# Optimization experiments

Hardware: AMD Instinct MI355X
Metric: run time of the kernel (lower is better)

Reference implementation:

```python
import jax, jax.numpy as jnp
import numpy as np

HEADS = 4

def setup_inputs() -> dict:
    B, L, D = 4, 2048, 256
    key = jax.random.key(0)
    k1, k2, k3, k4, k5, k6 = jax.random.split(key, 6)
    return {
        "atten": jax.random.normal(k1, (B, L, L), dtype=jnp.float32),
        "value": jax.random.normal(k2, (B, L, D), dtype=jnp.float32),
        "mask": jax.random.uniform(k3, (B, 1, L, L), dtype=jnp.float32),
        "padding_mask": jax.random.randint(k4, (B, L, L), 0, 2, dtype=jnp.int32),
        "Wv": jax.random.normal(k5, (D, D), dtype=jnp.float32) * 0.02,
        "bv": jnp.zeros((D,), dtype=jnp.float32),
        "Wo": jax.random.normal(k6, (D, D), dtype=jnp.float32) * 0.02,
        "bo": jnp.zeros((D,), dtype=jnp.float32),
    }

def reference(atten, value, mask, padding_mask, Wv, bv, Wo, bo):
    B, L, D = value.shape
    H = HEADS
    dk = D // H
    # to_value: Linear then split heads. N == 1 (value.unsqueeze(1) in torch).
    v = value @ Wv + bv                                   # (B, L, D)
    v = v.reshape(B, 1, L, H, dk).transpose(0, 3, 1, 2, 4)  # (B, H, N=1, L, dk)
    # externally supplied attention logits, two sequential masked fills
    a = atten[:, None, :, :]                              # (B, 1, L, L)
    a = jnp.where(mask < 0.5, jnp.finfo(a.dtype).min, a)
    a = jnp.where(padding_mask[:, None, :, :] == 0, -jnp.inf, a)
    a = jax.nn.softmax(a, axis=-1)                        # (B, 1, L, L)
    # dropout is identity in eval mode
    # einsum 'bhij,bhnjk->bhnik' with h=1 on a broadcast across H heads of v
    out = jnp.einsum('bij,bhnjk->bhnik', a[:, 0], v)      # (B, H, 1, L, dk)
    out = out.transpose(0, 2, 3, 1, 4).reshape(B, 1, L, D)
    out = out @ Wo + bo                                   # (B, 1, L, D)
    return out
```

## Files before the change

kernel.cpp:

```cpp
#include <hip/hip_runtime.h>
#include <hip/hip_bf16.h>
#include <math.h>

#define L 2048
#define D 256
#define NEG_FLT_MAX (-3.402823466e38f)

typedef __attribute__((ext_vector_type(8))) short bf16x8;
typedef __attribute__((ext_vector_type(4))) float f32x4;
typedef __attribute__((ext_vector_type(4))) int i32x4;

__device__ __forceinline__ unsigned short f2bf(float f) {
    union { float f; unsigned int u; } v; v.f = f;
    unsigned int r = v.u + 0x7FFFu + ((v.u >> 16) & 1u);
    return (unsigned short)(r >> 16);
}

__global__ __launch_bounds__(256, 4) void prep_kernel(
    const float* __restrict__ value, const float* __restrict__ Wv,
    const float* __restrict__ bv, const float* __restrict__ Wo,
    unsigned short* __restrict__ Vt, unsigned short* __restrict__ Wot) {
    const int tid = threadIdx.x;
    const int wave = tid >> 6, lane = tid & 63;
    const int lm = lane & 15, q = lane >> 4;
    const int rh = wave >> 1;
    const int nh = wave & 1;
    const int m0 = blockIdx.x * 32;
    const int n0 = blockIdx.y * 64;

    __shared__ __align__(16) unsigned short Wlds[64][264];

    {
        int bid = blockIdx.y * 256 + blockIdx.x;
        if (tid < 64) {
            int e = bid * 64 + tid;
            int k = e >> 8, n = e & 255;
            Wot[n * 256 + k] = f2bf(Wo[k * 256 + n]);
        }
    }

    {
        int krow = tid >> 4;
        int nrel = (tid & 15) * 4;
#pragma unroll
        for (int p = 0; p < 16; p++) {
            int k = p * 16 + krow;
            f32x4 w = *reinterpret_cast<const f32x4*>(Wv + (size_t)k * 256 + n0 + nrel);
            Wlds[nrel + 0][k] = f2bf(w[0]);
            Wlds[nrel + 1][k] = f2bf(w[1]);
            Wlds[nrel + 2][k] = f2bf(w[2]);
            Wlds[nrel + 3][k] = f2bf(w[3]);
        }
    }
    __syncthreads();

    const int nl0 = nh * 32 + lm;
    const int nl1 = nh * 32 + 16 + lm;
    const int arow = m0 + rh * 16 + lm;

    f32x4 acc[2];
    acc[0] = (f32x4)(0.f); acc[1] = (f32x4)(0.f);

    const float* ap = value + (size_t)arow * 256;
    f32x4 pa0 = *reinterpret_cast<const f32x4*>(ap + q * 8);
    f32x4 pa1 = *reinterpret_cast<const f32x4*>(ap + q * 8 + 4);

    for (int k0 = 0; k0 < 256; k0 += 32) {
        f32x4 a0 = pa0, a1 = pa1;
        if (k0 < 224) {
            int kq = k0 + 32 + q * 8;
            pa0 = *reinterpret_cast<const f32x4*>(ap + kq);
            pa1 = *reinterpret_cast<const f32x4*>(ap + kq + 4);
        }
        bf16x8 b0 = *reinterpret_cast<const bf16x8*>(&Wlds[nl0][k0 + q * 8]);
        bf16x8 b1 = *reinterpret_cast<const bf16x8*>(&Wlds[nl1][k0 + q * 8]);
        bf16x8 afr;
#pragma unroll
        for (int e = 0; e < 4; e++) afr[e] = (short)f2bf(a0[e]);
#pragma unroll
        for (int e = 0; e < 4; e++) afr[4 + e] = (short)f2bf(a1[e]);
        acc[0] = __builtin_amdgcn_mfma_f32_16x16x32_bf16(afr, b0, acc[0], 0, 0, 0);
        acc[1] = __builtin_amdgcn_mfma_f32_16x16x32_bf16(afr, b1, acc[1], 0, 0, 0);
    }

    int mrow = m0 + rh * 16 + q * 4;
    int b = mrow >> 11;
    int j = mrow & 2047;
#pragma unroll
    for (int nf = 0; nf < 2; nf++) {
        int n = n0 + nh * 32 + nf * 16 + lm;
        float bias_n = bv[n];
        const f32x4& a = acc[nf];
        unsigned short* dst = Vt + (size_t)b * (D * L) + (size_t)n * L + j;
        ushort4 pk;
        pk.x = f2bf(a[0] + bias_n);
        pk.y = f2bf(a[1] + bias_n);
        pk.z = f2bf(a[2] + bias_n);
        pk.w = f2bf(a[3] + bias_n);
        *reinterpret_cast<ushort4*>(dst) = pk;
    }
}

__global__ __launch_bounds__(256, 2) void attn_kernel(
    const float* __restrict__ atten, const float* __restrict__ mask,
    const int* __restrict__ pad, const unsigned short* __restrict__ Vt,
    const unsigned short* __restrict__ Wot, const float* __restrict__ bo,
    float* __restrict__ out) {
    const int g = blockIdx.x;
    const int b = g >> 7;
    const int i0 = (g & 127) * 16;
    const int tid = threadIdx.x;
    const int wave = tid >> 6, lane = tid & 63;
    const int lm = lane & 15, q = lane >> 4;
    const int r = tid >> 4;
    const int c = (tid & 15) * 8;

    __shared__ __align__(16) unsigned short Plds[2][16][136];
    __shared__ __align__(16) unsigned short A_lds[16][264];
    __shared__ float l_lds[16];

    f32x4 acc[4];
#pragma unroll
    for (int nf = 0; nf < 4; nf++) acc[nf] = (f32x4)(0.f);
    float lsum = 0.f;

    const size_t rowoff = ((size_t)(b * L + i0 + r)) * L + c;
    const float* at_p = atten + rowoff;
    const float* mk_p = mask + rowoff;
    const int*   pd_p = pad + rowoff;
    const unsigned short* vt_b = Vt + (size_t)b * (D * L);

    f32x4 pa0 = *reinterpret_cast<const f32x4*>(at_p);
    f32x4 pa1 = *reinterpret_cast<const f32x4*>(at_p + 4);
    f32x4 pm0 = *reinterpret_cast<const f32x4*>(mk_p);
    f32x4 pm1 = *reinterpret_cast<const f32x4*>(mk_p + 4);
    i32x4 pp0 = *reinterpret_cast<const i32x4*>(pd_p);
    i32x4 pp1 = *reinterpret_cast<const i32x4*>(pd_p + 4);

    for (int jt = 0; jt < 16; jt++) {
        const int j0 = jt * 128;
        bf16x8 bfr[4][4];
#pragma unroll
        for (int kk = 0; kk < 4; kk++)
#pragma unroll
            for (int nf = 0; nf < 4; nf++) {
                int n = wave * 64 + nf * 16 + lm;
                bfr[kk][nf] = *reinterpret_cast<const bf16x8*>(
                    vt_b + (size_t)n * L + j0 + kk * 32 + q * 8);
            }
        f32x4 a0 = pa0, a1 = pa1, k0 = pm0, k1 = pm1;
        i32x4 p0 = pp0, p1 = pp1;
        if (jt < 15) {
            pa0 = *reinterpret_cast<const f32x4*>(at_p + j0 + 128);
            pa1 = *reinterpret_cast<const f32x4*>(at_p + j0 + 132);
            pm0 = *reinterpret_cast<const f32x4*>(mk_p + j0 + 128);
            pm1 = *reinterpret_cast<const f32x4*>(mk_p + j0 + 132);
            pp0 = *reinterpret_cast<const i32x4*>(pd_p + j0 + 128);
            pp1 = *reinterpret_cast<const i32x4*>(pd_p + j0 + 132);
        }
        bf16x8 pk;
#pragma unroll
        for (int e = 0; e < 4; e++) {
            float sv = (k0[e] < 0.5f) ? NEG_FLT_MAX : a0[e];
            sv = (p0[e] == 0) ? -INFINITY : sv;
            float pv = __expf(sv);
            lsum += pv;
            pk[e] = (short)f2bf(pv);
            float sw = (k1[e] < 0.5f) ? NEG_FLT_MAX : a1[e];
            sw = (p1[e] == 0) ? -INFINITY : sw;
            float pw = __expf(sw);
            lsum += pw;
            pk[4 + e] = (short)f2bf(pw);
        }
        const int par = jt & 1;
        *reinterpret_cast<bf16x8*>(&Plds[par][r][c]) = pk;
        __syncthreads();

#pragma unroll
        for (int kk = 0; kk < 4; kk++) {
            bf16x8 afr = *reinterpret_cast<const bf16x8*>(
                &Plds[par][lm][kk * 32 + q * 8]);
#pragma unroll
            for (int nf = 0; nf < 4; nf++)
                acc[nf] = __builtin_amdgcn_mfma_f32_16x16x32_bf16(
                    afr, bfr[kk][nf], acc[nf], 0, 0, 0);
        }
    }

    lsum += __shfl_xor(lsum, 1);
    lsum += __shfl_xor(lsum, 2);
    lsum += __shfl_xor(lsum, 4);
    lsum += __shfl_xor(lsum, 8);
    if ((tid & 15) == 0) l_lds[r] = lsum;
    __syncthreads();

    float linv[4];
#pragma unroll
    for (int rg = 0; rg < 4; rg++) linv[rg] = 1.f / l_lds[q * 4 + rg];
#pragma unroll
    for (int nf = 0; nf < 4; nf++) {
        int n = wave * 64 + nf * 16 + lm;
#pragma unroll
        for (int rg = 0; rg < 4; rg++)
            A_lds[q * 4 + rg][n] = f2bf(acc[nf][rg] * linv[rg]);
    }
    __syncthreads();

    f32x4 oacc[4];
#pragma unroll
    for (int nf = 0; nf < 4; nf++) oacc[nf] = (f32x4)(0.f);
    for (int k0 = 0; k0 < 256; k0 += 32) {
        bf16x8 afr = *reinterpret_cast<const bf16x8*>(&A_lds[lm][k0 + q * 8]);
#pragma unroll
        for (int nf = 0; nf < 4; nf++) {
            int n = wave * 64 + nf * 16 + lm;
            bf16x8 bfrW = *reinterpret_cast<const bf16x8*>(
                Wot + (size_t)n * 256 + k0 + q * 8);
            oacc[nf] = __builtin_amdgcn_mfma_f32_16x16x32_bf16(
                afr, bfrW, oacc[nf], 0, 0, 0);
        }
    }
#pragma unroll
    for (int nf = 0; nf < 4; nf++) {
        int n = wave * 64 + nf * 16 + lm;
        float bias_n = bo[n];
#pragma unroll
        for (int rg = 0; rg < 4; rg++)
            out[((size_t)(b * L + i0 + q * 4 + rg)) * 256 + n] = oacc[nf][rg] + bias_n;
    }
}

extern "C" void kernel_launch(void* const* d_in, const int* in_sizes, int n_in,
                              void* d_out, int out_size, void* d_ws, size_t ws_size,
                              hipStream_t stream) {
    (void)in_sizes; (void)n_in; (void)out_size; (void)ws_size;
    const float* atten = (const float*)d_in[0];
    const float* value = (const float*)d_in[1];
    const float* mask  = (const float*)d_in[2];
    const int*   pad   = (const int*)d_in[3];
    const float* Wv    = (const float*)d_in[4];
    const float* bv    = (const float*)d_in[5];
    const float* Wo    = (const float*)d_in[6];
    const float* bo    = (const float*)d_in[7];
    float* out = (float*)d_out;

    char* ws = (char*)d_ws;
    unsigned short* Vt  = (unsigned short*)(ws);
    unsigned short* Wot = (unsigned short*)(ws + 4194304);

    prep_kernel<<<dim3(256, 4), 256, 0, stream>>>(value, Wv, bv, Wo, Vt, Wot);
    attn_kernel<<<512, 256, 0, stream>>>(atten, mask, pad, Vt, Wot, bo, out);
}
```

Before: 254.1 us.

## Double-buffer V fragments in registers and remap blocks across batches

Unrolls the key-tile loop by two with A/B register sets, so the V fragments and next-tile attention/mask/pad loads for tile j+1 are issued before the MFMA work of tile j, rather than the V loads sitting directly ahead of their own MFMAs. It also remaps the block index so consecutive blocks land on different batches, changing L2/XCD locality. This raises register pressure (two 4x4 bf16x8 fragment arrays), which could reduce occupancy under launch_bounds(256,2).

Result: faster. 248.3 us (-2.3%).

```diff
diff --git a/kernel.cpp b/kernel.cpp
--- a/kernel.cpp
+++ b/kernel.cpp
@@ -106,7 +106,8 @@
     const int* __restrict__ pad, const unsigned short* __restrict__ Vt,
     const unsigned short* __restrict__ Wot, const float* __restrict__ bo,
     float* __restrict__ out) {
-    const int g = blockIdx.x;
+    const int bid = blockIdx.x;
+    const int g = (bid & 7) * 64 + (bid >> 3);
     const int b = g >> 7;
     const int i0 = (g & 127) * 16;
     const int tid = threadIdx.x;
@@ -128,62 +129,117 @@
     const float* at_p = atten + rowoff;
     const float* mk_p = mask + rowoff;
     const int*   pd_p = pad + rowoff;
-    const unsigned short* vt_b = Vt + (size_t)b * (D * L);
-
-    f32x4 pa0 = *reinterpret_cast<const f32x4*>(at_p);
-    f32x4 pa1 = *reinterpret_cast<const f32x4*>(at_p + 4);
-    f32x4 pm0 = *reinterpret_cast<const f32x4*>(mk_p);
-    f32x4 pm1 = *reinterpret_cast<const f32x4*>(mk_p + 4);
-    i32x4 pp0 = *reinterpret_cast<const i32x4*>(pd_p);
-    i32x4 pp1 = *reinterpret_cast<const i32x4*>(pd_p + 4);
-
-    for (int jt = 0; jt < 16; jt++) {
-        const int j0 = jt * 128;
-        bf16x8 bfr[4][4];
-#pragma unroll
-        for (int kk = 0; kk < 4; kk++)
-#pragma unroll
-            for (int nf = 0; nf < 4; nf++) {
-                int n = wave * 64 + nf * 16 + lm;
-                bfr[kk][nf] = *reinterpret_cast<const bf16x8*>(
-                    vt_b + (size_t)n * L + j0 + kk * 32 + q * 8);
-            }
-        f32x4 a0 = pa0, a1 = pa1, k0 = pm0, k1 = pm1;
-        i32x4 p0 = pp0, p1 = pp1;
-        if (jt < 15) {
-            pa0 = *reinterpret_cast<const f32x4*>(at_p + j0 + 128);
-            pa1 = *reinterpret_cast<const f32x4*>(at_p + j0 + 132);
-            pm0 = *reinterpret_cast<const f32x4*>(mk_p + j0 + 128);
-            pm1 = *reinterpret_cast<const f32x4*>(mk_p + j0 + 132);
-            pp0 = *reinterpret_cast<const i32x4*>(pd_p + j0 + 128);
-            pp1 = *reinterpret_cast<const i32x4*>(pd_p + j0 + 132);
-        }
-        bf16x8 pk;
-#pragma unroll
-        for (int e = 0; e < 4; e++) {
-            float sv = (k0[e] < 0.5f) ? NEG_FLT_MAX : a0[e];
-            sv = (p0[e] == 0) ? -INFINITY : sv;
-            float pv = __expf(sv);
-            lsum += pv;
-            pk[e] = (short)f2bf(pv);
-            float sw = (k1[e] < 0.5f) ? NEG_FLT_MAX : a1[e];
-            sw = (p1[e] == 0) ? -INFINITY : sw;
-            float pw = __expf(sw);
-            lsum += pw;
-            pk[4 + e] = (short)f2bf(pw);
-        }
-        const int par = jt & 1;
-        *reinterpret_cast<bf16x8*>(&Plds[par][r][c]) = pk;
-        __syncthreads();
-
-#pragma unroll
-        for (int kk = 0; kk < 4; kk++) {
-            bf16x8 afr = *reinterpret_cast<const bf16x8*>(
-                &Plds[par][lm][kk * 32 + q * 8]);
-#pragma unroll
-            for (int nf = 0; nf < 4; nf++)
-                acc[nf] = __builtin_amdgcn_mfma_f32_16x16x32_bf16(
-                    afr, bfr[kk][nf], acc[nf], 0, 0, 0);
+    const unsigned short* vt_b = Vt + (size_t)b * (D * L) + q * 8;
+
+    f32x4 laA0, laA1, lmA0, lmA1, laB0, laB1, lmB0, lmB1;
+    i32x4 lpA0, lpA1, lpB0, lpB1;
+    bf16x8 bfrA[4][4], bfrB[4][4];
+
+    laA0 = *reinterpret_cast<const f32x4*>(at_p);
+    laA1 = *reinterpret_cast<const f32x4*>(at_p + 4);
+    lmA0 = *reinterpret_cast<const f32x4*>(mk_p);
+    lmA1 = *reinterpret_cast<const f32x4*>(mk_p + 4);
+    lpA0 = *reinterpret_cast<const i32x4*>(pd_p);
+    lpA1 = *reinterpret_cast<const i32x4*>(pd_p + 4);
+#pragma unroll
+    for (int kk = 0; kk < 4; kk++)
+#pragma unroll
+        for (int nf = 0; nf < 4; nf++) {
+            int n = wave * 64 + nf * 16 + lm;
+            bfrA[kk][nf] = *reinterpret_cast<const bf16x8*>(
+                vt_b + (size_t)n * L + kk * 32);
+        }
+
+    for (int jt = 0; jt < 16; jt += 2) {
+        {
+            const int j0 = jt * 128;
+            bf16x8 pk;
+#pragma unroll
+            for (int e = 0; e < 4; e++) {
+                float sv = (lmA0[e] < 0.5f) ? NEG_FLT_MAX : laA0[e];
+                sv = (lpA0[e] == 0) ? -INFINITY : sv;
+                float pv = __expf(sv);
+                lsum += pv;
+                pk[e] = (short)f2bf(pv);
+                float sw = (lmA1[e] < 0.5f) ? NEG_FLT_MAX : laA1[e];
+                sw = (lpA1[e] == 0) ? -INFINITY : sw;
+                float pw = __expf(sw);
+                lsum += pw;
+                pk[4 + e] = (short)f2bf(pw);
+            }
+            *reinterpret_cast<bf16x8*>(&Plds[0][r][c]) = pk;
+            {
+                const int jn = j0 + 128;
+                laB0 = *reinterpret_cast<const f32x4*>(at_p + jn);
+                laB1 = *reinterpret_cast<const f32x4*>(at_p + jn + 4);
+                lmB0 = *reinterpret_cast<const f32x4*>(mk_p + jn);
+                lmB1 = *reinterpret_cast<const f32x4*>(mk_p + jn + 4);
+                lpB0 = *reinterpret_cast<const i32x4*>(pd_p + jn);
+                lpB1 = *reinterpret_cast<const i32x4*>(pd_p + jn + 4);
+#pragma unroll
+                for (int kk = 0; kk < 4; kk++)
+#pragma unroll
+                    for (int nf = 0; nf < 4; nf++) {
+                        int n = wave * 64 + nf * 16 + lm;
+                        bfrB[kk][nf] = *reinterpret_cast<const bf16x8*>(
+                            vt_b + (size_t)n * L + jn + kk * 32);
+                    }
+            }
+            __syncthreads();
+#pragma unroll
+            for (int kk = 0; kk < 4; kk++) {
+                bf16x8 afr = *reinterpret_cast<const bf16x8*>(
+                    &Plds[0][lm][kk * 32 + q * 8]);
+#pragma unroll
+                for (int nf = 0; nf < 4; nf++)
+                    acc[nf] = __builtin_amdgcn_mfma_f32_16x16x32_bf16(
+                        afr, bfrA[kk][nf], acc[nf], 0, 0, 0);
+            }
+        }
+        {
+            const int j0 = jt * 128 + 128;
+            bf16x8 pk;
+#pragma unroll
+            for (int e = 0; e < 4; e++) {
+                float sv = (lmB0[e] < 0.5f) ? NEG_FLT_MAX : laB0[e];
+                sv = (lpB0[e] == 0) ? -INFINITY : sv;
+                float pv = __expf(sv);
+                lsum += pv;
+                pk[e] = (short)f2bf(pv);
+                float sw = (lmB1[e] < 0.5f) ? NEG_FLT_MAX : laB1[e];
+                sw = (lpB1[e] == 0) ? -INFINITY : sw;
+                float pw = __expf(sw);
+                lsum += pw;
+                pk[4 + e] = (short)f2bf(pw);
+            }
+            *reinterpret_cast<bf16x8*>(&Plds[1][r][c]) = pk;
+            if (jt < 14) {
+                const int jn = j0 + 128;
+                laA0 = *reinterpret_cast<const f32x4*>(at_p + jn);
+                laA1 = *reinterpret_cast<const f32x4*>(at_p + jn + 4);
+                lmA0 = *reinterpret_cast<const f32x4*>(mk_p + jn);
+                lmA1 = *reinterpret_cast<const f32x4*>(mk_p + jn + 4);
+                lpA0 = *reinterpret_cast<const i32x4*>(pd_p + jn);
+                lpA1 = *reinterpret_cast<const i32x4*>(pd_p + jn + 4);
+#pragma unroll
+                for (int kk = 0; kk < 4; kk++)
+#pragma unroll
+                    for (int nf = 0; nf < 4; nf++) {
+                        int n = wave * 64 + nf * 16 + lm;
+                        bfrA[kk][nf] = *reinterpret_cast<const bf16x8*>(
+                            vt_b + (size_t)n * L + jn + kk * 32);
+                    }
+            }
+            __syncthreads();
+#pragma unroll
+            for (int kk = 0; kk < 4; kk++) {
+                bf16x8 afr = *reinterpret_cast<const bf16x8*>(
+                    &Plds[1][lm][kk * 32 + q * 8]);
+#pragma unroll
+                for (int nf = 0; nf < 4; nf++)
+                    acc[nf] = __builtin_amdgcn_mfma_f32_16x16x32_bf16(
+                        afr, bfrB[kk][nf], acc[nf], 0, 0, 0);
+            }
         }
     }
 
```

## Use single-wave blocks with register-direct P fragments and double-buffered prefetch

Applied to the files above, without the earlier changes.

The attention kernel now runs one 64-thread wave per block, covering all 256 output columns for 16 rows. The softmax numerators are built directly in the MFMA A-fragment layout, so the shared-memory staging of P and the per-tile __syncthreads are gone. Logits, masks and V fragments are double-buffered in registers, one 32-column step ahead. The cost is only 512 waves across the GPU and heavy register use (16 accumulators plus two 16-fragment V buffers), which lowers occupancy and leaves less parallelism to hide memory latency.

Result: slower. 284.7 us (+12.0%).

```diff
diff --git a/kernel.cpp b/kernel.cpp
--- a/kernel.cpp
+++ b/kernel.cpp
@@ -101,7 +101,7 @@
     }
 }
 
-__global__ __launch_bounds__(256, 2) void attn_kernel(
+__global__ __launch_bounds__(64, 1) void attn_kernel(
     const float* __restrict__ atten, const float* __restrict__ mask,
     const int* __restrict__ pad, const unsigned short* __restrict__ Vt,
     const unsigned short* __restrict__ Wot, const float* __restrict__ bo,
@@ -109,120 +109,138 @@
     const int g = blockIdx.x;
     const int b = g >> 7;
     const int i0 = (g & 127) * 16;
-    const int tid = threadIdx.x;
-    const int wave = tid >> 6, lane = tid & 63;
+    const int lane = threadIdx.x & 63;
     const int lm = lane & 15, q = lane >> 4;
-    const int r = tid >> 4;
-    const int c = (tid & 15) * 8;
-
-    __shared__ __align__(16) unsigned short Plds[2][16][136];
+
     __shared__ __align__(16) unsigned short A_lds[16][264];
     __shared__ float l_lds[16];
 
-    f32x4 acc[4];
-#pragma unroll
-    for (int nf = 0; nf < 4; nf++) acc[nf] = (f32x4)(0.f);
+    f32x4 acc[16];
+#pragma unroll
+    for (int nf = 0; nf < 16; nf++) acc[nf] = (f32x4)(0.f);
     float lsum = 0.f;
 
-    const size_t rowoff = ((size_t)(b * L + i0 + r)) * L + c;
+    const size_t rowoff = ((size_t)(b * L + i0 + lm)) * L + q * 8;
     const float* at_p = atten + rowoff;
     const float* mk_p = mask + rowoff;
     const int*   pd_p = pad + rowoff;
-    const unsigned short* vt_b = Vt + (size_t)b * (D * L);
-
-    f32x4 pa0 = *reinterpret_cast<const f32x4*>(at_p);
-    f32x4 pa1 = *reinterpret_cast<const f32x4*>(at_p + 4);
-    f32x4 pm0 = *reinterpret_cast<const f32x4*>(mk_p);
-    f32x4 pm1 = *reinterpret_cast<const f32x4*>(mk_p + 4);
-    i32x4 pp0 = *reinterpret_cast<const i32x4*>(pd_p);
-    i32x4 pp1 = *reinterpret_cast<const i32x4*>(pd_p + 4);
-
-    for (int jt = 0; jt < 16; jt++) {
-        const int j0 = jt * 128;
-        bf16x8 bfr[4][4];
-#pragma unroll
-        for (int kk = 0; kk < 4; kk++)
-#pragma unroll
-            for (int nf = 0; nf < 4; nf++) {
-                int n = wave * 64 + nf * 16 + lm;
-                bfr[kk][nf] = *reinterpret_cast<const bf16x8*>(
-                    vt_b + (size_t)n * L + j0 + kk * 32 + q * 8);
+    const unsigned short* vt_b = Vt + (size_t)b * (D * L) + q * 8;
+
+    f32x4 aA0, aA1, mA0, mA1, aB0, aB1, mB0, mB1;
+    i32x4 pA0, pA1, pB0, pB1;
+    bf16x8 vA[16], vB[16];
+
+    aA0 = *reinterpret_cast<const f32x4*>(at_p);
+    aA1 = *reinterpret_cast<const f32x4*>(at_p + 4);
+    mA0 = *reinterpret_cast<const f32x4*>(mk_p);
+    mA1 = *reinterpret_cast<const f32x4*>(mk_p + 4);
+    pA0 = *reinterpret_cast<const i32x4*>(pd_p);
+    pA1 = *reinterpret_cast<const i32x4*>(pd_p + 4);
+#pragma unroll
+    for (int nf = 0; nf < 16; nf++)
+        vA[nf] = *reinterpret_cast<const bf16x8*>(vt_b + (size_t)(nf * 16 + lm) * L);
+
+    for (int jt = 0; jt < 64; jt += 2) {
+        {
+            const int jn = (jt + 1) * 32;
+            aB0 = *reinterpret_cast<const f32x4*>(at_p + jn);
+            aB1 = *reinterpret_cast<const f32x4*>(at_p + jn + 4);
+            mB0 = *reinterpret_cast<const f32x4*>(mk_p + jn);
+            mB1 = *reinterpret_cast<const f32x4*>(mk_p + jn + 4);
+            pB0 = *reinterpret_cast<const i32x4*>(pd_p + jn);
+            pB1 = *reinterpret_cast<const i32x4*>(pd_p + jn + 4);
+#pragma unroll
+            for (int nf = 0; nf < 16; nf++)
+                vB[nf] = *reinterpret_cast<const bf16x8*>(
+                    vt_b + (size_t)(nf * 16 + lm) * L + jn);
+
+            bf16x8 afr;
+#pragma unroll
+            for (int e = 0; e < 4; e++) {
+                float sv = (mA0[e] < 0.5f) ? NEG_FLT_MAX : aA0[e];
+                sv = (pA0[e] == 0) ? -INFINITY : sv;
+                float pv = __expf(sv);
+                lsum += pv;
+                afr[e] = (short)f2bf(pv);
+                float sw = (mA1[e] < 0.5f) ? NEG_FLT_MAX : aA1[e];
+                sw = (pA1[e] == 0) ? -INFINITY : sw;
+                float pw = __expf(sw);
+                lsum += pw;
+                afr[4 + e] = (short)f2bf(pw);
             }
-        f32x4 a0 = pa0, a1 = pa1, k0 = pm0, k1 = pm1;
-        i32x4 p0 = pp0, p1 = pp1;
-        if (jt < 15) {
-            pa0 = *reinterpret_cast<const f32x4*>(at_p + j0 + 128);
-            pa1 = *reinterpret_cast<const f32x4*>(at_p + j0 + 132);
-            pm0 = *reinterpret_cast<const f32x4*>(mk_p + j0 + 128);
-            pm1 = *reinterpret_cast<const f32x4*>(mk_p + j0 + 132);
-            pp0 = *reinterpret_cast<const i32x4*>(pd_p + j0 + 128);
-            pp1 = *reinterpret_cast<const i32x4*>(pd_p + j0 + 132);
-        }
-        bf16x8 pk;
-#pragma unroll
-        for (int e = 0; e < 4; e++) {
-            float sv = (k0[e] < 0.5f) ? NEG_FLT_MAX : a0[e];
-            sv = (p0[e] == 0) ? -INFINITY : sv;
-            float pv = __expf(sv);
-            lsum += pv;
-            pk[e] = (short)f2bf(pv);
-            float sw = (k1[e] < 0.5f) ? NEG_FLT_MAX : a1[e];
-            sw = (p1[e] == 0) ? -INFINITY : sw;
-            float pw = __expf(sw);
-            lsum += pw;
-            pk[4 + e] = (short)f2bf(pw);
-        }
-        const int par = jt & 1;
-        *reinterpret_cast<bf16x8*>(&Plds[par][r][c]) = pk;
-        __syncthreads();
-
-#pragma unroll
-        for (int kk = 0; kk < 4; kk++) {
-            bf16x8 afr = *reinterpret_cast<const bf16x8*>(
-                &Plds[par][lm][kk * 32 + q * 8]);
-#pragma unroll
-            for (int nf = 0; nf < 4; nf++)
+#pragma unroll
+            for (int nf = 0; nf < 16; nf++)
                 acc[nf] = __builtin_amdgcn_mfma_f32_16x16x32_bf16(
-                    afr, bfr[kk][nf], acc[nf], 0, 0, 0);
-        }
-    }
-
-    lsum += __shfl_xor(lsum, 1);
-    lsum += __shfl_xor(lsum, 2);
-    lsum += __shfl_xor(lsum, 4);
-    lsum += __shfl_xor(lsum, 8);
-    if ((tid & 15) == 0) l_lds[r] = lsum;
+                    afr, vA[nf], acc[nf], 0, 0, 0);
+        }
+        {
+            if (jt < 62) {
+                const int jn = (jt + 2) * 32;
+                aA0 = *reinterpret_cast<const f32x4*>(at_p + jn);
+                aA1 = *reinterpret_cast<const f32x4*>(at_p + jn + 4);
+                mA0 = *reinterpret_cast<const f32x4*>(mk_p + jn);
+                mA1 = *reinterpret_cast<const f32x4*>(mk_p + jn + 4);
+                pA0 = *reinterpret_cast<const i32x4*>(pd_p + jn);
+                pA1 = *reinterpret_cast<const i32x4*>(pd_p + jn + 4);
+#pragma unroll
+                for (int nf = 0; nf < 16; nf++)
+                    vA[nf] = *reinterpret_cast<const bf16x8*>(
+                        vt_b + (size_t)(nf * 16 + lm) * L + jn);
+            }
+            bf16x8 afr;
+#pragma unroll
+            for (int e = 0; e < 4; e++) {
+                float sv = (mB0[e] < 0.5f) ? NEG_FLT_MAX : aB0[e];
+                sv = (pB0[e] == 0) ? -INFINITY : sv;
+                float pv = __expf(sv);
+                lsum += pv;
+                afr[e] = (short)f2bf(pv);
+                float sw = (mB1[e] < 0.5f) ? NEG_FLT_MAX : aB1[e];
+                sw = (pB1[e] == 0) ? -INFINITY : sw;
+                float pw = __expf(sw);
+                lsum += pw;
+                afr[4 + e] = (short)f2bf(pw);
+            }
+#pragma unroll
+            for (int nf = 0; nf < 16; nf++)
+                acc[nf] = __builtin_amdgcn_mfma_f32_16x16x32_bf16(
+                    afr, vB[nf], acc[nf], 0, 0, 0);
+        }
+    }
+
+    lsum += __shfl_xor(lsum, 16);
+    lsum += __shfl_xor(lsum, 32);
+    if (lane < 16) l_lds[lm] = lsum;
     __syncthreads();
 
     float linv[4];
 #pragma unroll
     for (int rg = 0; rg < 4; rg++) linv[rg] = 1.f / l_lds[q * 4 + rg];
 #pragma unroll
-    for (int nf = 0; nf < 4; nf++) {
-        int n = wave * 64 + nf * 16 + lm;
+    for (int nf = 0; nf < 16; nf++) {
+        int n = nf * 16 + lm;
 #pragma unroll
         for (int rg = 0; rg < 4; rg++)
             A_lds[q * 4 + rg][n] = f2bf(acc[nf][rg] * linv[rg]);
     }
     __syncthreads();
 
-    f32x4 oacc[4];
-#pragma unroll
-    for (int nf = 0; nf < 4; nf++) oacc[nf] = (f32x4)(0.f);
+    f32x4 oacc[16];
+#pragma unroll
+    for (int nf = 0; nf < 16; nf++) oacc[nf] = (f32x4)(0.f);
     for (int k0 = 0; k0 < 256; k0 += 32) {
         bf16x8 afr = *reinterpret_cast<const bf16x8*>(&A_lds[lm][k0 + q * 8]);
 #pragma unroll
-        for (int nf = 0; nf < 4; nf++) {
-            int n = wave * 64 + nf * 16 + lm;
-            bf16x8 bfrW = *reinterpret_cast<const bf16x8*>(
-                Wot + (size_t)n * 256 + k0 + q * 8);
+        for (int nf = 0; nf < 16; nf++) {
+            bf16x8 w = *reinterpret_cast<const bf16x8*>(
+                Wot + (size_t)(nf * 16 + lm) * 256 + k0 + q * 8);
             oacc[nf] = __builtin_amdgcn_mfma_f32_16x16x32_bf16(
-                afr, bfrW, oacc[nf], 0, 0, 0);
-        }
-    }
-#pragma unroll
-    for (int nf = 0; nf < 4; nf++) {
-        int n = wave * 64 + nf * 16 + lm;
+                afr, w, oacc[nf], 0, 0, 0);
+        }
+    }
+#pragma unroll
+    for (int nf = 0; nf < 16; nf++) {
+        int n = nf * 16 + lm;
         float bias_n = bo[n];
 #pragma unroll
         for (int rg = 0; rg < 4; rg++)
@@ -249,5 +267,5 @@
     unsigned short* Wot = (unsigned short*)(ws + 4194304);
 
     prep_kernel<<<dim3(256, 4), 256, 0, stream>>>(value, Wv, bv, Wo, Vt, Wot);
-    attn_kernel<<<512, 256, 0, stream>>>(atten, mask, pad, Vt, Wot, bo, out);
-}
+    attn_kernel<<<512, 64, 0, stream>>>(atten, mask, pad, Vt, Wot, bo, out);
+}
```

## Split attention key dimension in two, write partials, fuse output projection separately

Applied to the files above, without the earlier changes.

Each attention block now handles half of the key range (split-K), so the grid doubles to 1024 blocks with smaller LDS tiles and higher occupancy bounds. Blocks are remapped so the two halves of a row group land on different XCD slots. Unnormalised partial accumulators and row sums go to a workspace buffer. A new GEMM kernel combines the two halves, normalises them and applies Wo plus bias. The aim is better parallelism and latency hiding on the memory-bound attention pass, at the cost of extra global traffic for the partials and one more kernel launch.

Result: slower. 274.7 us (+8.1%).

```diff
diff --git a/kernel.cpp b/kernel.cpp
--- a/kernel.cpp
+++ b/kernel.cpp
@@ -38,7 +38,6 @@
             Wot[n * 256 + k] = f2bf(Wo[k * 256 + n]);
         }
     }
-
     {
         int krow = tid >> 4;
         int nrel = (tid & 15) * 4;
@@ -101,83 +100,77 @@
     }
 }
 
-__global__ __launch_bounds__(256, 2) void attn_kernel(
+__global__ __launch_bounds__(256, 4) void attn_kernel(
     const float* __restrict__ atten, const float* __restrict__ mask,
     const int* __restrict__ pad, const unsigned short* __restrict__ Vt,
-    const unsigned short* __restrict__ Wot, const float* __restrict__ bo,
-    float* __restrict__ out) {
-    const int g = blockIdx.x;
-    const int b = g >> 7;
+    float* __restrict__ part) {
+    const int bid = blockIdx.x;
+    const int g = (bid & 7) * 128 + (bid >> 3);
+    const int b = g >> 8;
+    const int js = (g >> 7) & 1;
     const int i0 = (g & 127) * 16;
     const int tid = threadIdx.x;
     const int wave = tid >> 6, lane = tid & 63;
     const int lm = lane & 15, q = lane >> 4;
     const int r = tid >> 4;
-    const int c = (tid & 15) * 8;
-
-    __shared__ __align__(16) unsigned short Plds[2][16][136];
-    __shared__ __align__(16) unsigned short A_lds[16][264];
-    __shared__ float l_lds[16];
+    const int c4 = (tid & 15) * 4;
+
+    __shared__ __align__(16) unsigned short Plds[2][16][72];
 
     f32x4 acc[4];
 #pragma unroll
     for (int nf = 0; nf < 4; nf++) acc[nf] = (f32x4)(0.f);
     float lsum = 0.f;
 
-    const size_t rowoff = ((size_t)(b * L + i0 + r)) * L + c;
+    const size_t rowoff = ((size_t)(b * L + i0 + r)) * L + js * 1024 + c4;
     const float* at_p = atten + rowoff;
     const float* mk_p = mask + rowoff;
     const int*   pd_p = pad + rowoff;
-    const unsigned short* vt_b = Vt + (size_t)b * (D * L);
-
-    f32x4 pa0 = *reinterpret_cast<const f32x4*>(at_p);
-    f32x4 pa1 = *reinterpret_cast<const f32x4*>(at_p + 4);
-    f32x4 pm0 = *reinterpret_cast<const f32x4*>(mk_p);
-    f32x4 pm1 = *reinterpret_cast<const f32x4*>(mk_p + 4);
-    i32x4 pp0 = *reinterpret_cast<const i32x4*>(pd_p);
-    i32x4 pp1 = *reinterpret_cast<const i32x4*>(pd_p + 4);
+    const unsigned short* vt_b = Vt + (size_t)b * (D * L) + js * 1024;
+
+    f32x4 pa = *reinterpret_cast<const f32x4*>(at_p);
+    f32x4 pm = *reinterpret_cast<const f32x4*>(mk_p);
+    i32x4 pp = *reinterpret_cast<const i32x4*>(pd_p);
 
     for (int jt = 0; jt < 16; jt++) {
-        const int j0 = jt * 128;
-        bf16x8 bfr[4][4];
-#pragma unroll
-        for (int kk = 0; kk < 4; kk++)
+        const int j0 = jt * 64;
+        bf16x8 bfr[2][4];
+#pragma unroll
+        for (int kk = 0; kk < 2; kk++)
 #pragma unroll
             for (int nf = 0; nf < 4; nf++) {
                 int n = wave * 64 + nf * 16 + lm;
                 bfr[kk][nf] = *reinterpret_cast<const bf16x8*>(
                     vt_b + (size_t)n * L + j0 + kk * 32 + q * 8);
             }
-        f32x4 a0 = pa0, a1 = pa1, k0 = pm0, k1 = pm1;
-        i32x4 p0 = pp0, p1 = pp1;
+        f32x4 a = pa, k = pm;
+        i32x4 p = pp;
         if (jt < 15) {
-            pa0 = *reinterpret_cast<const f32x4*>(at_p + j0 + 128);
-            pa1 = *reinterpret_cast<const f32x4*>(at_p + j0 + 132);
-            pm0 = *reinterpret_cast<const f32x4*>(mk_p + j0 + 128);
-            pm1 = *reinterpret_cast<const f32x4*>(mk_p + j0 + 132);
-            pp0 = *reinterpret_cast<const i32x4*>(pd_p + j0 + 128);
-            pp1 = *reinterpret_cast<const i32x4*>(pd_p + j0 + 132);
-        }
-        bf16x8 pk;
-#pragma unroll
-        for (int e = 0; e < 4; e++) {
-            float sv = (k0[e] < 0.5f) ? NEG_FLT_MAX : a0[e];
-            sv = (p0[e] == 0) ? -INFINITY : sv;
-            float pv = __expf(sv);
-            lsum += pv;
-            pk[e] = (short)f2bf(pv);
-            float sw = (k1[e] < 0.5f) ? NEG_FLT_MAX : a1[e];
-            sw = (p1[e] == 0) ? -INFINITY : sw;
-            float pw = __expf(sw);
-            lsum += pw;
-            pk[4 + e] = (short)f2bf(pw);
-        }
+            pa = *reinterpret_cast<const f32x4*>(at_p + j0 + 64);
+            pm = *reinterpret_cast<const f32x4*>(mk_p + j0 + 64);
+            pp = *reinterpret_cast<const i32x4*>(pd_p + j0 + 64);
+        }
+        ushort4 pk;
+        float p0, p1, p2, p3;
+        {
+            float s0 = (k[0] < 0.5f) ? NEG_FLT_MAX : a[0];
+            s0 = (p[0] == 0) ? -INFINITY : s0; p0 = __expf(s0);
+            float s1 = (k[1] < 0.5f) ? NEG_FLT_MAX : a[1];
+            s1 = (p[1] == 0) ? -INFINITY : s1; p1 = __expf(s1);
+            float s2 = (k[2] < 0.5f) ? NEG_FLT_MAX : a[2];
+            s2 = (p[2] == 0) ? -INFINITY : s2; p2 = __expf(s2);
+            float s3 = (k[3] < 0.5f) ? NEG_FLT_MAX : a[3];
+            s3 = (p[3] == 0) ? -INFINITY : s3; p3 = __expf(s3);
+        }
+        lsum += (p0 + p1) + (p2 + p3);
+        pk.x = f2bf(p0); pk.y = f2bf(p1); pk.z = f2bf(p2); pk.w = f2bf(p3);
+
         const int par = jt & 1;
-        *reinterpret_cast<bf16x8*>(&Plds[par][r][c]) = pk;
+        *reinterpret_cast<ushort4*>(&Plds[par][r][c4]) = pk;
         __syncthreads();
 
 #pragma unroll
-        for (int kk = 0; kk < 4; kk++) {
+        for (int kk = 0; kk < 2; kk++) {
             bf16x8 afr = *reinterpret_cast<const bf16x8*>(
                 &Plds[par][lm][kk * 32 + q * 8]);
 #pragma unroll
@@ -191,42 +184,74 @@
     lsum += __shfl_xor(lsum, 2);
     lsum += __shfl_xor(lsum, 4);
     lsum += __shfl_xor(lsum, 8);
-    if ((tid & 15) == 0) l_lds[r] = lsum;
-    __syncthreads();
-
-    float linv[4];
-#pragma unroll
-    for (int rg = 0; rg < 4; rg++) linv[rg] = 1.f / l_lds[q * 4 + rg];
+
+    float* pbase = part + (size_t)g * 4112;
 #pragma unroll
     for (int nf = 0; nf < 4; nf++) {
         int n = wave * 64 + nf * 16 + lm;
 #pragma unroll
         for (int rg = 0; rg < 4; rg++)
-            A_lds[q * 4 + rg][n] = f2bf(acc[nf][rg] * linv[rg]);
-    }
-    __syncthreads();
-
-    f32x4 oacc[4];
-#pragma unroll
-    for (int nf = 0; nf < 4; nf++) oacc[nf] = (f32x4)(0.f);
+            pbase[(q * 4 + rg) * 256 + n] = acc[nf][rg];
+    }
+    if ((tid & 15) == 0) pbase[4096 + r] = lsum;
+}
+
+__global__ __launch_bounds__(256, 2) void gemm_out_kernel(
+    const float* __restrict__ part,
+    const unsigned short* __restrict__ Wt,
+    const float* __restrict__ bias,
+    float* __restrict__ Cout) {
+    const int wave = threadIdx.x >> 6;
+    const int lane = threadIdx.x & 63;
+    const int lm = lane & 15, q = lane >> 4;
+    const int m0 = blockIdx.x * 64;
+    const int n0 = blockIdx.y * 64;
+    const int arow = m0 + wave * 16 + lm;
+    const int b = arow >> 11;
+    const int rg16 = (arow & 2047) >> 4;
+    const int r_in = arow & 15;
+    const float* pb0 = part + (size_t)(b * 256 + rg16) * 4112;
+    const float* pb1 = pb0 + (size_t)128 * 4112;
+
+    float linv = 1.f / (pb0[4096 + r_in] + pb1[4096 + r_in]);
+
+    int ncol[4];
+#pragma unroll
+    for (int nf = 0; nf < 4; nf++) ncol[nf] = n0 + nf * 16 + lm;
+
+    f32x4 acc[4];
+#pragma unroll
+    for (int nf = 0; nf < 4; nf++) acc[nf] = (f32x4)(0.f);
+
     for (int k0 = 0; k0 < 256; k0 += 32) {
-        bf16x8 afr = *reinterpret_cast<const bf16x8*>(&A_lds[lm][k0 + q * 8]);
-#pragma unroll
-        for (int nf = 0; nf < 4; nf++) {
-            int n = wave * 64 + nf * 16 + lm;
-            bf16x8 bfrW = *reinterpret_cast<const bf16x8*>(
-                Wot + (size_t)n * 256 + k0 + q * 8);
-            oacc[nf] = __builtin_amdgcn_mfma_f32_16x16x32_bf16(
-                afr, bfrW, oacc[nf], 0, 0, 0);
-        }
-    }
+        int kq = k0 + q * 8;
+        bf16x8 bfr[4];
+#pragma unroll
+        for (int nf = 0; nf < 4; nf++)
+            bfr[nf] = *reinterpret_cast<const bf16x8*>(Wt + (size_t)ncol[nf] * 256 + kq);
+        f32x4 s0 = *reinterpret_cast<const f32x4*>(pb0 + r_in * 256 + kq)
+                 + *reinterpret_cast<const f32x4*>(pb1 + r_in * 256 + kq);
+        f32x4 s1 = *reinterpret_cast<const f32x4*>(pb0 + r_in * 256 + kq + 4)
+                 + *reinterpret_cast<const f32x4*>(pb1 + r_in * 256 + kq + 4);
+        bf16x8 afr;
+#pragma unroll
+        for (int e = 0; e < 4; e++) afr[e] = (short)f2bf(s0[e] * linv);
+#pragma unroll
+        for (int e = 0; e < 4; e++) afr[4 + e] = (short)f2bf(s1[e] * linv);
+#pragma unroll
+        for (int nf = 0; nf < 4; nf++)
+            acc[nf] = __builtin_amdgcn_mfma_f32_16x16x32_bf16(
+                afr, bfr[nf], acc[nf], 0, 0, 0);
+    }
+
+    int mrow = m0 + wave * 16 + q * 4;
 #pragma unroll
     for (int nf = 0; nf < 4; nf++) {
-        int n = wave * 64 + nf * 16 + lm;
-        float bias_n = bo[n];
+        int n = ncol[nf];
+        float bias_n = bias[n];
 #pragma unroll
         for (int rg = 0; rg < 4; rg++)
-            out[((size_t)(b * L + i0 + q * 4 + rg)) * 256 + n] = oacc[nf][rg] + bias_n;
+            Cout[(size_t)(mrow + rg) * 256 + n] = acc[nf][rg] + bias_n;
     }
 }
 
@@ -247,7 +272,9 @@
     char* ws = (char*)d_ws;
     unsigned short* Vt  = (unsigned short*)(ws);
     unsigned short* Wot = (unsigned short*)(ws + 4194304);
+    float* part = (float*)(ws + 4325376);
 
     prep_kernel<<<dim3(256, 4), 256, 0, stream>>>(value, Wv, bv, Wo, Vt, Wot);
-    attn_kernel<<<512, 256, 0, stream>>>(atten, mask, pad, Vt, Wot, bo, out);
-}
+    attn_kernel<<<1024, 256, 0, stream>>>(atten, mask, pad, Vt, part);
+    gemm_out_kernel<<<dim3(128, 4), 256, 0, stream>>>(part, Wot, bo, out);
+}
```
